# Kernel tuning notes

Hardware: AMD Instinct MI355X
Metric: run time of the kernel (lower is better)

Reference implementation:

```python
import jax, jax.numpy as jnp
import numpy as np

B, S, D_IN, H, D_HEAD = 8, 1024, 768, 12, 64

def setup_inputs() -> dict:
    key = jax.random.key(0)
    k1, k2, k3, k4 = jax.random.split(key, 4)
    x = jax.random.normal(k1, (B, S, D_IN), dtype=jnp.float32)
    # per-head projection weights, stacked: [H, d_in, d_head]
    scale = 1.0 / np.sqrt(D_IN)
    Wq = jax.random.normal(k2, (H, D_IN, D_HEAD), dtype=jnp.float32) * scale
    Wk = jax.random.normal(k3, (H, D_IN, D_HEAD), dtype=jnp.float32) * scale
    Wv = jax.random.normal(k4, (H, D_IN, D_HEAD), dtype=jnp.float32) * scale
    return {"x": x, "Wq": Wq, "Wk": Wk, "Wv": Wv}

def reference(x, Wq, Wk, Wv) -> jnp.ndarray:
    # Batched equivalent of the Python loop over heads + concat.
    q = jnp.einsum('bsd,hde->bhse', x, Wq)  # [B,H,S,Dh]
    k = jnp.einsum('bsd,hde->bhse', x, Wk)
    v = jnp.einsum('bsd,hde->bhse', x, Wv)
    scores = jnp.einsum('bhse,bhte->bhst', q, k) / jnp.sqrt(jnp.asarray(D_HEAD, x.dtype))
    causal = jnp.tril(jnp.ones((S, S), dtype=bool))  # [S,S]
    scores = jnp.where(causal, scores, jnp.asarray(-jnp.inf, x.dtype))
    attn = jax.nn.softmax(scores, axis=-1)  # dropout p=0.0 -> identity
    ctx = jnp.einsum('bhst,bhte->bhse', attn, v)  # [B,H,S,Dh]
    # concat heads along last dim -> [B,S,H*Dh]
    return jnp.transpose(ctx, (0, 2, 1, 3)).reshape(B, S, H * D_HEAD)
```

## Files before the change

kernel.cpp:

```cpp
#include <hip/hip_runtime.h>

typedef short short8 __attribute__((ext_vector_type(8)));
typedef float f32x4 __attribute__((ext_vector_type(4)));
typedef float f32x16 __attribute__((ext_vector_type(16)));

#define SQ   1024
#define DIN  768
#define NH   12
#define DH   64
#define SCL2 0.1803368801111243f

static __device__ __forceinline__ ushort f2bf(float f) {
  union { float f; unsigned u; } v; v.f = f;
  unsigned u = v.u;
  unsigned r = (u + 0x7FFFu + ((u >> 16) & 1u)) >> 16;
  return (ushort)r;
}
static __device__ __forceinline__ unsigned pk2(float a, float b) {
  return (unsigned)f2bf(a) | ((unsigned)f2bf(b) << 16);
}

static __device__ __forceinline__ void gload_lds16(const ushort* g, ushort* l) {
  __builtin_amdgcn_global_load_lds(
      (const __attribute__((address_space(1))) unsigned*)(g),
      (__attribute__((address_space(3))) unsigned*)(l),
      16, 0, 0);
}

__global__ __launch_bounds__(256) void k_convert_x(const float* __restrict__ x,
                                                   ushort* __restrict__ xb) {
  int i = (blockIdx.x * 256 + threadIdx.x) * 4;
  float4 v = *reinterpret_cast<const float4*>(x + i);
  ushort4 o;
  o.x = f2bf(v.x); o.y = f2bf(v.y); o.z = f2bf(v.z); o.w = f2bf(v.w);
  *reinterpret_cast<ushort4*>(xb + i) = o;
}

__global__ __launch_bounds__(256) void k_prep_w(const float* __restrict__ Wq,
                                                const float* __restrict__ Wk,
                                                const float* __restrict__ Wv,
                                                ushort* __restrict__ wt) {
  __shared__ ushort tile[64][65];
  const int mh = blockIdx.x;
  const int m = mh / 12, h = mh % 12;
  const int d0 = blockIdx.y * 64;
  const float* W = (m == 0 ? Wq : (m == 1 ? Wk : Wv)) + h * DIN * DH;
  ushort* outp = wt + (size_t)mh * DH * DIN;
  #pragma unroll
  for (int p = 0; p < 16; ++p) {
    int idx = p * 256 + threadIdx.x;
    int d = idx >> 6, e = idx & 63;
    tile[d][e] = f2bf(W[(d0 + d) * DH + e]);
  }
  __syncthreads();
  #pragma unroll
  for (int p = 0; p < 16; ++p) {
    int idx = p * 256 + threadIdx.x;
    int e = idx >> 6, d = idx & 63;
    outp[e * DIN + d0 + d] = tile[d][e];
  }
}

__global__ __launch_bounds__(256) void k_proj(const ushort* __restrict__ xb,
                                              const ushort* __restrict__ wt,
                                              ushort* __restrict__ qo,
                                              ushort* __restrict__ ko,
                                              ushort* __restrict__ vto) {
  __shared__ __align__(16) ushort Ab[2][128][32];
  __shared__ __align__(16) ushort Bb[2][128][32];

  const int brow = blockIdx.x * 128;
  const int bn   = blockIdx.y * 128;
  const int w    = threadIdx.x >> 6, lane = threadIdx.x & 63;
  const int lr   = lane & 15, lg = lane >> 4;
  const int wm   = w >> 1, wn = w & 1;

  const int srow  = threadIdx.x >> 2;
  const int sslot = (threadIdx.x & 3) ^ (srow & 3);
  const ushort* gA = xb + (size_t)(brow + srow) * DIN + sslot * 8;
  const ushort* gB = wt + (size_t)(bn   + srow) * DIN + sslot * 8;
  ushort* lA = &Ab[0][0][0] + threadIdx.x * 8;
  ushort* lB = &Bb[0][0][0] + threadIdx.x * 8;

  f32x4 acc[4][4];
  #pragma unroll
  for (int i = 0; i < 4; ++i)
    #pragma unroll
    for (int j = 0; j < 4; ++j) acc[i][j] = (f32x4){0.f, 0.f, 0.f, 0.f};

  const int aslot = (lg ^ (lr & 3)) * 8;

  gload_lds16(gA,            lA);
  gload_lds16(gA + 64 * DIN, lA + 2048);
  gload_lds16(gB,            lB);
  gload_lds16(gB + 64 * DIN, lB + 2048);
  __syncthreads();

  int cur = 0;
  #pragma unroll 1
  for (int t = 0; t < 24; ++t) {
    if (t + 1 < 24) {
      const int k0 = (t + 1) * 32;
      const int nb = (cur ^ 1) * 4096;
      gload_lds16(gA + k0,            lA + nb);
      gload_lds16(gA + k0 + 64 * DIN, lA + nb + 2048);
      gload_lds16(gB + k0,            lB + nb);
      gload_lds16(gB + k0 + 64 * DIN, lB + nb + 2048);
    }
    short8 a[4], b[4];
    #pragma unroll
    for (int mi = 0; mi < 4; ++mi)
      a[mi] = *reinterpret_cast<const short8*>(&Ab[cur][wm * 64 + mi * 16 + lr][aslot]);
    #pragma unroll
    for (int ci = 0; ci < 4; ++ci)
      b[ci] = *reinterpret_cast<const short8*>(&Bb[cur][wn * 64 + ci * 16 + lr][aslot]);
    #pragma unroll
    for (int mi = 0; mi < 4; ++mi)
      #pragma unroll
      for (int ci = 0; ci < 4; ++ci)
        acc[mi][ci] = __builtin_amdgcn_mfma_f32_16x16x32_bf16(a[mi], b[ci], acc[mi][ci], 0, 0, 0);
    __syncthreads();
    cur ^= 1;
  }

  const int mh = (bn + wn * 64) >> 6;
  const int m = mh / 12, h = mh % 12;
  #pragma unroll
  for (int mi = 0; mi < 4; ++mi)
    #pragma unroll
    for (int ci = 0; ci < 4; ++ci)
      #pragma unroll
      for (int r = 0; r < 4; ++r) {
        int rg = brow + wm * 64 + mi * 16 + lg * 4 + r;
        int b_ = rg >> 10, sl = rg & 1023;
        int bh = b_ * 12 + h;
        int e  = ci * 16 + lr;
        ushort val = f2bf(acc[mi][ci][r]);
        if (m == 2) {
          vto[((size_t)bh * DH + e) * SQ + sl] = val;
        } else {
          ushort* dst = (m == 0) ? qo : ko;
          dst[((size_t)bh * SQ + sl) * DH + e] = val;
        }
      }
}

__global__ __launch_bounds__(256, 3) void k_attn(const ushort* __restrict__ qi,
                                                 const ushort* __restrict__ ki,
                                                 const ushort* __restrict__ vti,
                                                 float* __restrict__ out) {
  __shared__ __align__(16) ushort Kb[2][64 * 64];
  __shared__ __align__(16) ushort Vb[2][64 * 64];

  const int f = blockIdx.x;
  const int g = f >> 8, r_ = f & 255;
  const int qt = ((r_ & 7) + g * 3) & 7;
  const int bh = g * 32 + (r_ >> 3);
  const int b = bh / 12, h = bh % 12;
  const int w = threadIdx.x >> 6, lane = threadIdx.x & 63;
  const int ql = lane & 31, hi = lane >> 5;
  const int q0 = qt * 128 + w * 32;
  const int nt = (q0 >> 6) + 1;
  const int ntmax = 2 * qt + 2;
  const ushort* qb = qi  + (size_t)bh * SQ * DH;
  const ushort* kb = ki  + (size_t)bh * SQ * DH;
  const ushort* vb = vti + (size_t)bh * DH * SQ;

  short8 qf[4];
  #pragma unroll
  for (int m = 0; m < 4; ++m)
    qf[m] = *reinterpret_cast<const short8*>(qb + (size_t)(q0 + ql) * DH + m * 16 + hi * 8);

  f32x16 o0, o1;
  #pragma unroll
  for (int r = 0; r < 16; ++r) { o0[r] = 0.f; o1[r] = 0.f; }
  float m_run = -1e30f, l_run = 0.f;

#define STAGE(bufi, tt) do {                                                                   \
    const int kv0_ = (tt) * 64;                                                                \
    const int t0 = threadIdx.x, t1 = threadIdx.x + 256;                                        \
    gload_lds16(kb + (size_t)(kv0_ + (t0 >> 3)) * DH + (((t0 & 7) ^ ((t0 >> 3) & 7)) * 8),     \
                &Kb[bufi][0] + t0 * 8);                                                        \
    gload_lds16(kb + (size_t)(kv0_ + (t1 >> 3)) * DH + (((t1 & 7) ^ ((t1 >> 3) & 7)) * 8),     \
                &Kb[bufi][0] + t1 * 8);                                                        \
    gload_lds16(vb + (size_t)(t0 >> 3) * SQ + kv0_ + (((t0 & 7) ^ ((t0 >> 3) & 7)) * 8),       \
                &Vb[bufi][0] + t0 * 8);                                                        \
    gload_lds16(vb + (size_t)(t1 >> 3) * SQ + kv0_ + (((t1 & 7) ^ ((t1 >> 3) & 7)) * 8),       \
                &Vb[bufi][0] + t1 * 8);                                                        \
  } while (0)

  STAGE(0, 0);
  __syncthreads();

  int cur = 0;
  #pragma unroll 1
  for (int t = 0; t < ntmax; ++t) {
    if (t + 1 < ntmax) STAGE(cur ^ 1, t + 1);

    if (t < nt) {
      const int kv0 = t * 64;
      const ushort* Kc = &Kb[cur][0];
      const ushort* Vc = &Vb[cur][0];

      f32x16 s0, s1;
      #pragma unroll
      for (int r = 0; r < 16; ++r) { s0[r] = 0.f; s1[r] = 0.f; }
      #pragma unroll
      for (int m = 0; m < 4; ++m) {
        short8 kf = *reinterpret_cast<const short8*>(Kc + ql * 64 + ((2 * m + hi) ^ (ql & 7)) * 8);
        s0 = __builtin_amdgcn_mfma_f32_32x32x16_bf16(kf, qf[m], s0, 0, 0, 0);
      }
      #pragma unroll
      for (int m = 0; m < 4; ++m) {
        short8 kf = *reinterpret_cast<const short8*>(Kc + (32 + ql) * 64 + ((2 * m + hi) ^ (ql & 7)) * 8);
        s1 = __builtin_amdgcn_mfma_f32_32x32x16_bf16(kf, qf[m], s1, 0, 0, 0);
      }

      if (t == nt - 1) {
        const int qg = q0 + ql;
        #pragma unroll
        for (int r = 0; r < 16; ++r) {
          int kvl = (r & 3) + 8 * (r >> 2) + 4 * hi;
          if (kv0 + kvl      > qg) s0[r] = -1e30f;
          if (kv0 + 32 + kvl > qg) s1[r] = -1e30f;
        }
      }

      float mt = s0[0];
      #pragma unroll
      for (int r = 1; r < 16; ++r) mt = fmaxf(mt, s0[r]);
      #pragma unroll
      for (int r = 0; r < 16; ++r) mt = fmaxf(mt, s1[r]);
      mt = fmaxf(mt, __shfl_xor(mt, 32));
      if (__any(mt > m_run + 40.0f)) {
        float mnew = fmaxf(m_run, mt);
        float corr = exp2f((m_run - mnew) * SCL2);
        l_run *= corr; m_run = mnew;
        #pragma unroll
        for (int r = 0; r < 16; ++r) {
          float cr = __shfl(corr, (r & 3) + 8 * (r >> 2) + 4 * hi);
          o0[r] *= cr; o1[r] *= cr;
        }
      }
      float ts = 0.f;
      #pragma unroll
      for (int r = 0; r < 16; ++r) {
        s0[r] = exp2f((s0[r] - m_run) * SCL2); ts += s0[r];
        s1[r] = exp2f((s1[r] - m_run) * SCL2); ts += s1[r];
      }
      ts += __shfl_xor(ts, 32);
      l_run += ts;

#define PV_CHUNK(SV, CC, KC) do {                                                              \
        unsigned wa = pk2(SV[(CC) * 8 + 0], SV[(CC) * 8 + 1]);                                 \
        unsigned wb = pk2(SV[(CC) * 8 + 2], SV[(CC) * 8 + 3]);                                 \
        unsigned wc = pk2(SV[(CC) * 8 + 4], SV[(CC) * 8 + 5]);                                 \
        unsigned wd = pk2(SV[(CC) * 8 + 6], SV[(CC) * 8 + 7]);                                 \
        unsigned xa = __shfl_xor(wa, 32), xb2 = __shfl_xor(wb, 32);                            \
        unsigned xc = __shfl_xor(wc, 32), xd = __shfl_xor(wd, 32);                             \
        uint4 pw;                                                                              \
        pw.x = hi ? xc : wa;  pw.y = hi ? xd : wb;                                             \
        pw.z = hi ? wc : xa;  pw.w = hi ? wd : xb2;                                            \
        short8 pa = *reinterpret_cast<short8*>(&pw);                                           \
        short8 vf0 = *reinterpret_cast<const short8*>(Vc + ql * 64 +                           \
                       ((2 * (KC) + hi) ^ (ql & 7)) * 8);                                      \
        o0 = __builtin_amdgcn_mfma_f32_32x32x16_bf16(pa, vf0, o0, 0, 0, 0);                    \
        short8 vf1 = *reinterpret_cast<const short8*>(Vc + (32 + ql) * 64 +                    \
                       ((2 * (KC) + hi) ^ (ql & 7)) * 8);                                      \
        o1 = __builtin_amdgcn_mfma_f32_32x32x16_bf16(pa, vf1, o1, 0, 0, 0);                    \
      } while (0)

      PV_CHUNK(s0, 0, 0);
      PV_CHUNK(s0, 1, 1);
      PV_CHUNK(s1, 0, 2);
      PV_CHUNK(s1, 1, 3);
#undef PV_CHUNK
    }

    __syncthreads();
    cur ^= 1;
  }
#undef STAGE

  float rl = 1.0f / l_run;
  #pragma unroll
  for (int r = 0; r < 16; ++r) {
    int base = (r & 3) + 8 * (r >> 2) + 4 * hi;
    float sc_ = __shfl(rl, base);
    int qg = q0 + base;
    float* op = out + ((size_t)b * SQ + qg) * (NH * DH) + h * DH;
    op[ql]      = o0[r] * sc_;
    op[32 + ql] = o1[r] * sc_;
  }
}

extern "C" void kernel_launch(void* const* d_in, const int* in_sizes, int n_in,
                              void* d_out, int out_size, void* d_ws, size_t ws_size,
                              hipStream_t stream) {
  const float* x  = (const float*)d_in[0];
  const float* Wq = (const float*)d_in[1];
  const float* Wk = (const float*)d_in[2];
  const float* Wv = (const float*)d_in[3];
  float* out = (float*)d_out;

  char* ws = (char*)d_ws;
  ushort* xb = (ushort*)(ws);
  ushort* wt = (ushort*)(ws + 12582912);
  ushort* q  = (ushort*)(ws + 16121856);
  ushort* k  = (ushort*)(ws + 28704768);
  ushort* vt = (ushort*)(ws + 41287680);

  k_convert_x<<<6144, 256, 0, stream>>>(x, xb);
  k_prep_w<<<dim3(36, 12), 256, 0, stream>>>(Wq, Wk, Wv, wt);
  k_proj<<<dim3(64, 18), 256, 0, stream>>>(xb, wt, q, k, vt);
  k_attn<<<768, 256, 0, stream>>>(q, k, vt, out);
}
```

Before: 198.0 us.

## Triple-buffer projection GEMM LDS with vmcnt waits and stronger swizzle

Measured after the change: 199.8 us. About the same (+0.9%).

```diff
diff --git a/kernel.cpp b/kernel.cpp
--- a/kernel.cpp
+++ b/kernel.cpp
@@ -66,8 +66,8 @@
                                               ushort* __restrict__ qo,
                                               ushort* __restrict__ ko,
                                               ushort* __restrict__ vto) {
-  __shared__ __align__(16) ushort Ab[2][128][32];
-  __shared__ __align__(16) ushort Bb[2][128][32];
+  __shared__ __align__(16) ushort Ab[3][128][32];
+  __shared__ __align__(16) ushort Bb[3][128][32];
 
   const int brow = blockIdx.x * 128;
   const int bn   = blockIdx.y * 128;
@@ -76,11 +76,9 @@
   const int wm   = w >> 1, wn = w & 1;
 
   const int srow  = threadIdx.x >> 2;
-  const int sslot = (threadIdx.x & 3) ^ (srow & 3);
+  const int sslot = (threadIdx.x & 3) ^ (srow & 3) ^ ((srow >> 2) & 3);
   const ushort* gA = xb + (size_t)(brow + srow) * DIN + sslot * 8;
   const ushort* gB = wt + (size_t)(bn   + srow) * DIN + sslot * 8;
-  ushort* lA = &Ab[0][0][0] + threadIdx.x * 8;
-  ushort* lB = &Bb[0][0][0] + threadIdx.x * 8;
 
   f32x4 acc[4][4];
   #pragma unroll
@@ -88,50 +86,63 @@
     #pragma unroll
     for (int j = 0; j < 4; ++j) acc[i][j] = (f32x4){0.f, 0.f, 0.f, 0.f};
 
-  const int aslot = (lg ^ (lr & 3)) * 8;
-
-  gload_lds16(gA,            lA);
-  gload_lds16(gA + 64 * DIN, lA + 2048);
-  gload_lds16(gB,            lB);
-  gload_lds16(gB + 64 * DIN, lB + 2048);
-  __syncthreads();
+  const int fr   = (lr & 3) ^ ((lr >> 2) & 3);
+  const int aoff = (lg ^ fr) * 8;
+
+#define STAGE(bi, tt) do {                                                \
+    const int k0_ = (tt) * 32;                                            \
+    ushort* la_ = &Ab[bi][0][0] + threadIdx.x * 8;                        \
+    ushort* lb_ = &Bb[bi][0][0] + threadIdx.x * 8;                        \
+    gload_lds16(gA + k0_,            la_);                                \
+    gload_lds16(gA + k0_ + 64 * DIN, la_ + 2048);                         \
+    gload_lds16(gB + k0_,            lb_);                                \
+    gload_lds16(gB + k0_ + 64 * DIN, lb_ + 2048);                         \
+  } while (0)
+
+  STAGE(0, 0);
+  STAGE(1, 1);
 
   int cur = 0;
   #pragma unroll 1
   for (int t = 0; t < 24; ++t) {
-    if (t + 1 < 24) {
-      const int k0 = (t + 1) * 32;
-      const int nb = (cur ^ 1) * 4096;
-      gload_lds16(gA + k0,            lA + nb);
-      gload_lds16(gA + k0 + 64 * DIN, lA + nb + 2048);
-      gload_lds16(gB + k0,            lB + nb);
-      gload_lds16(gB + k0 + 64 * DIN, lB + nb + 2048);
+    if (t < 23) {
+      asm volatile("s_waitcnt vmcnt(4)" ::: "memory");
+    } else {
+      asm volatile("s_waitcnt vmcnt(0)" ::: "memory");
+    }
+    __builtin_amdgcn_sched_barrier(0);
+    __builtin_amdgcn_s_barrier();
+    __builtin_amdgcn_sched_barrier(0);
+    if (t + 2 < 24) {
+      int nb = cur + 2; if (nb >= 3) nb -= 3;
+      STAGE(nb, t + 2);
     }
     short8 a[4], b[4];
     #pragma unroll
     for (int mi = 0; mi < 4; ++mi)
-      a[mi] = *reinterpret_cast<const short8*>(&Ab[cur][wm * 64 + mi * 16 + lr][aslot]);
+      a[mi] = *reinterpret_cast<const short8*>(&Ab[cur][wm * 64 + mi * 16 + lr][aoff]);
     #pragma unroll
     for (int ci = 0; ci < 4; ++ci)
-      b[ci] = *reinterpret_cast<const short8*>(&Bb[cur][wn * 64 + ci * 16 + lr][aslot]);
+      b[ci] = *reinterpret_cast<const short8*>(&Bb[cur][wn * 64 + ci * 16 + lr][aoff]);
     #pragma unroll
     for (int mi = 0; mi < 4; ++mi)
       #pragma unroll
       for (int ci = 0; ci < 4; ++ci)
         acc[mi][ci] = __builtin_amdgcn_mfma_f32_16x16x32_bf16(a[mi], b[ci], acc[mi][ci], 0, 0, 0);
-    __syncthreads();
-    cur ^= 1;
-  }
+    cur += 1; if (cur >= 3) cur = 0;
+  }
+#undef STAGE
 
   const int mh = (bn + wn * 64) >> 6;
   const int m = mh / 12, h = mh % 12;
+  const int lgq = lane >> 4;
   #pragma unroll
   for (int mi = 0; mi < 4; ++mi)
     #pragma unroll
     for (int ci = 0; ci < 4; ++ci)
       #pragma unroll
       for (int r = 0; r < 4; ++r) {
-        int rg = brow + wm * 64 + mi * 16 + lg * 4 + r;
+        int rg = brow + wm * 64 + mi * 16 + lgq * 4 + r;
         int b_ = rg >> 10, sl = rg & 1023;
         int bh = b_ * 12 + h;
         int e  = ci * 16 + lr;
```
